# Performance work log

Measured on AMD Instinct MI355X. Metric: run time of the kernel, lower is better.

## Reference

```python
import jax, jax.numpy as jnp
import numpy as np

B, S, D_IN, D_OUT = 4, 2048, 1024, 64
USE_MASK = True

def setup_inputs() -> dict:
    key = jax.random.key(0)
    ks = jax.random.split(key, 6)
    return {
        "inputs_for_keys": jax.random.normal(ks[0], (B, S, D_IN), jnp.float32),
        "inputs_for_values": jax.random.normal(ks[1], (B, S, D_IN), jnp.float32),
        "inputs_for_queries": jax.random.normal(ks[2], (B, S, D_IN), jnp.float32),
        "Weight_Q": jax.random.normal(ks[3], (D_IN, D_OUT), jnp.float32) * 0.02,
        "Weight_K": jax.random.normal(ks[4], (D_IN, D_OUT), jnp.float32) * 0.02,
        "Weight_V": jax.random.normal(ks[5], (D_IN, D_OUT), jnp.float32) * 0.02,
    }

def reference(inputs_for_keys, inputs_for_values, inputs_for_queries, Weight_Q, Weight_K, Weight_V):
    Q = jnp.einsum('bsd,de->bse', inputs_for_queries, Weight_Q)
    K = jnp.einsum('bsd,de->bse', inputs_for_keys, Weight_K)
    V = jnp.einsum('bsd,de->bse', inputs_for_values, Weight_V)
    # scores: [B, S_q, S_k], scaled by sqrt(d_out)
    scores = jnp.einsum('bqe,bke->bqk', Q, K) / np.sqrt(D_OUT).astype(np.float32)
    if USE_MASK:
        # -inf strictly above the diagonal (causal mask), matching
        # transpose(tril(ones*-inf, -1)) in the original.
        q_idx = jnp.arange(S)[:, None]
        k_idx = jnp.arange(S)[None, :]
        scores = jnp.where(k_idx > q_idx, -jnp.inf, scores)
    attn = jax.nn.softmax(scores, axis=-1)
    return jnp.einsum('bqk,bke->bqe', attn, V)
```

## Files before the change

### kernel.cpp

```cpp
#include <hip/hip_runtime.h>
#include <hip/hip_bf16.h>
#include <stdint.h>

typedef __bf16 bf16_t;
typedef __bf16 bf16x8 __attribute__((ext_vector_type(8)));
typedef float f32x4 __attribute__((ext_vector_type(4)));

#define L2E 1.44269504088896340736f

static __device__ __forceinline__ f32x4 mfma16(bf16x8 a, bf16x8 b, f32x4 c) {
  return __builtin_amdgcn_mfma_f32_16x16x32_bf16(a, b, c, 0, 0, 0);
}

static __device__ __forceinline__ void gload_lds16(const void* g, void* l) {
  __builtin_amdgcn_global_load_lds(
      (const __attribute__((address_space(1))) uint32_t*)g,
      (__attribute__((address_space(3))) uint32_t*)l, 16, 0, 0);
}

static __device__ __forceinline__ float bf2f(uint16_t u) {
  union { uint32_t i; float f; } v; v.i = (uint32_t)u << 16; return v.f;
}

__global__ __launch_bounds__(256) void wt_kernel(const float* __restrict__ Wq,
                                                 const float* __restrict__ Wk,
                                                 const float* __restrict__ Wv,
                                                 bf16_t* __restrict__ Wt) {
  int gid = blockIdx.x * 256 + threadIdx.x;
  int proj = gid >> 16;
  int rem = gid & 65535;
  int k = rem >> 6, n = rem & 63;
  const float* W = (proj == 0) ? Wq : (proj == 1) ? Wk : Wv;
  float v = W[rem];
  if (proj == 0) v *= 0.125f;
  Wt[proj * 65536 + n * 1024 + k] = (bf16_t)v;
}

__global__ __launch_bounds__(512) void proj_kernel(
    const float* __restrict__ Xq, const float* __restrict__ Xk, const float* __restrict__ Xv,
    const bf16_t* __restrict__ Wt,
    bf16_t* __restrict__ Qb, bf16_t* __restrict__ Kb, bf16_t* __restrict__ Vt) {
  __shared__ alignas(16) char Xl[8 * 4096];
  __shared__ alignas(16) bf16_t Msm[8][16][64];

  int tid = threadIdx.x;
  int w = tid >> 6, lane = tid & 63;
  int l15 = lane & 15, g = lane >> 4;
  char* myx = Xl + w * 4096;
  int kw = w;

  bf16x8 Wf[4][4];

  auto loadW = [&](int p) {
    const char* wb = (const char*)Wt + (size_t)p * 131072 + (size_t)kw * 256;
#pragma unroll
    for (int ct = 0; ct < 4; ++ct) {
#pragma unroll
      for (int i = 0; i < 4; ++i) {
        int n = i * 4 + (lane >> 4);
        int srcb = ((lane & 15) * 16) ^ ((n & 7) << 4);
        gload_lds16(wb + (size_t)(ct * 16 + n) * 2048 + srcb, myx + i * 1024);
      }
      asm volatile("s_waitcnt vmcnt(0)" ::: "memory");
      __builtin_amdgcn_sched_barrier(0);
#pragma unroll
      for (int s2 = 0; s2 < 4; ++s2)
        Wf[ct][s2] = *(const bf16x8*)(myx + l15 * 256 + ((s2 * 64 + g * 16) ^ ((l15 & 7) << 4)));
      asm volatile("s_waitcnt lgkmcnt(0)" ::: "memory");
      __builtin_amdgcn_sched_barrier(0);
    }
  };

  f32x4 acc[4] = {};
  float4 xA[4], xB[4];

  auto issueX = [&](int t, int sub, float4* xr) {
    int p = t >> 9, lt = t & 511;
    const float* X = (p == 0) ? Xq : (p == 1) ? Xk : Xv;
    const float* base = X + (size_t)lt * 16384 + kw * 128 + sub * 64 + (lane & 15) * 4;
#pragma unroll
    for (int i = 0; i < 4; ++i)
      xr[i] = *(const float4*)(base + ((lane >> 4) + 4 * i) * 1024);
  };

  auto writeX = [&](const float4* xr, int sub) {
    char* buf = myx + sub * 2048;
#pragma unroll
    for (int i = 0; i < 4; ++i) {
      int rw = (lane >> 4) + 4 * i;
      bf16_t t4[4] = {(bf16_t)xr[i].x, (bf16_t)xr[i].y, (bf16_t)xr[i].z, (bf16_t)xr[i].w};
      *(uint2*)(buf + rw * 128 + (((lane & 15) * 8) ^ ((rw & 7) << 4))) = *(const uint2*)t4;
    }
    asm volatile("s_waitcnt lgkmcnt(0)" ::: "memory");
    __builtin_amdgcn_sched_barrier(0);
  };

  auto computeX = [&](int sub) {
    const char* buf = myx + sub * 2048;
#pragma unroll
    for (int ks = 0; ks < 2; ++ks) {
      bf16x8 af = *(const bf16x8*)(buf + l15 * 128 + ((ks * 64 + g * 16) ^ ((l15 & 7) << 4)));
#pragma unroll
      for (int ct = 0; ct < 4; ++ct)
        acc[ct] = mfma16(af, Wf[ct][sub * 2 + ks], acc[ct]);
    }
  };

  int t0 = blockIdx.x * 6;
  int cur_p = t0 >> 9;
  loadW(cur_p);
  issueX(t0, 0, xA);

#pragma unroll 1
  for (int T = 0; T < 6; ++T) {
    int t = t0 + T;
    int p = t >> 9, lt = t & 511;
    if (p != cur_p) { loadW(p); cur_p = p; }
    issueX(t, 1, xB);
    writeX(xA, 0);
    computeX(0);
    if (T < 5) issueX(t + 1, 0, xA);
    writeX(xB, 1);
    computeX(1);

#pragma unroll
    for (int ct = 0; ct < 4; ++ct)
#pragma unroll
      for (int r = 0; r < 4; ++r)
        Msm[w][g * 4 + r][ct * 16 + l15] = (bf16_t)acc[ct][r];
#pragma unroll
    for (int ct = 0; ct < 4; ++ct) acc[ct] = (f32x4){0.f, 0.f, 0.f, 0.f};
    __syncthreads();

    int row = tid >> 5, c0 = (tid & 31) * 2;
    float s0 = 0.f, s1 = 0.f;
#pragma unroll
    for (int w2 = 0; w2 < 8; ++w2) {
      uint32_t u = *(const uint32_t*)&Msm[w2][row][c0];
      s0 += bf2f((uint16_t)u);
      s1 += bf2f((uint16_t)(u >> 16));
    }

    if (p < 2) {
      bf16_t* Ob = (p == 0) ? Qb : Kb;
      bf16_t o2[2] = {(bf16_t)s0, (bf16_t)s1};
      *(uint32_t*)&Ob[(size_t)(lt * 16 + row) * 64 + c0] = *(const uint32_t*)o2;
      __syncthreads();
    } else {
      __syncthreads();
      bf16_t* Vsm = (bf16_t*)&Msm[0][0][0];
      bf16_t o2[2] = {(bf16_t)s0, (bf16_t)s1};
      *(uint32_t*)&Vsm[row * 72 + c0] = *(const uint32_t*)o2;
      __syncthreads();
      if (tid < 128) {
        int d = tid >> 1, h = tid & 1;
        int b = lt >> 7;
        int s_ = (lt & 127) * 16 + h * 8;
        bf16_t tmp[8];
#pragma unroll
        for (int i = 0; i < 8; ++i) tmp[i] = Vsm[(h * 8 + i) * 72 + d];
        *(uint4*)(Vt + ((size_t)(b * 64 + d)) * 2048 + s_) = *(const uint4*)tmp;
      }
      __syncthreads();
    }
  }
}

#define NW 8
__global__ __launch_bounds__(512) void attn_kernel(
    const bf16_t* __restrict__ Qb, const bf16_t* __restrict__ Kb,
    const bf16_t* __restrict__ Vt, float* __restrict__ Out) {
  __shared__ alignas(16) char Psm[NW * 2048];
  __shared__ float accL[NW][16][64];
  __shared__ float mL[NW][16];
  __shared__ float lL[NW][16];

  int b = blockIdx.y;
  int x = blockIdx.x;
  int qt = (b >= 2) ? (127 - x) : x;
  int q0 = qt * 16;
  int tid = threadIdx.x;
  int w = tid >> 6, lane = tid & 63;
  int l15 = lane & 15, g = lane >> 4;
  char* Pw = Psm + w * 2048;

  size_t qrow = (size_t)(b * 2048 + q0 + l15) * 64;
  bf16x8 qf0 = *(const bf16x8*)(Qb + qrow + g * 8);
  bf16x8 qf1 = *(const bf16x8*)(Qb + qrow + 32 + g * 8);

  float m_run[4] = {-1e30f, -1e30f, -1e30f, -1e30f};
  float l_run[4] = {0.f, 0.f, 0.f, 0.f};
  f32x4 acc_o[4] = {};

  int ntiles = (q0 + 79) >> 6;
  const bf16_t* kbase = Kb + (size_t)b * 2048 * 64;
  const bf16_t* vbase = Vt + (size_t)b * 64 * 2048;

  for (int t = w; t < ntiles; t += NW) {
    int kv0 = t * 64;
    f32x4 s[4] = {};
#pragma unroll
    for (int ct = 0; ct < 4; ++ct) {
      const bf16_t* kr = kbase + (size_t)(kv0 + ct * 16 + l15) * 64 + g * 8;
      s[ct] = mfma16(qf0, *(const bf16x8*)kr, s[ct]);
      s[ct] = mfma16(qf1, *(const bf16x8*)(kr + 32), s[ct]);
    }
    if (t == ntiles - 1) {
#pragma unroll
      for (int ct = 0; ct < 4; ++ct)
#pragma unroll
        for (int r = 0; r < 4; ++r) {
          int kg_ = kv0 + ct * 16 + l15;
          int qg_ = q0 + g * 4 + r;
          if (kg_ > qg_) s[ct][r] = -1e30f;
        }
    }

#pragma unroll
    for (int r = 0; r < 4; ++r) {
      float mx = fmaxf(fmaxf(s[0][r], s[1][r]), fmaxf(s[2][r], s[3][r]));
      mx = fmaxf(mx, __shfl_xor(mx, 1, 64));
      mx = fmaxf(mx, __shfl_xor(mx, 2, 64));
      mx = fmaxf(mx, __shfl_xor(mx, 4, 64));
      mx = fmaxf(mx, __shfl_xor(mx, 8, 64));
      float mnew = fmaxf(m_run[r], mx);
      float scale = exp2f((m_run[r] - mnew) * L2E);
      m_run[r] = mnew;
      float ps = 0.f;
      int qrl = g * 4 + r;
      char* pb = Pw + qrl * 128;
      int swp = (qrl & 7) << 4;
#pragma unroll
      for (int ct = 0; ct < 4; ++ct) {
        float p = exp2f((s[ct][r] - mnew) * L2E);
        ps += p;
        *(bf16_t*)(pb + ((ct * 32 + l15 * 2) ^ swp)) = (bf16_t)p;
      }
      ps += __shfl_xor(ps, 1, 64);
      ps += __shfl_xor(ps, 2, 64);
      ps += __shfl_xor(ps, 4, 64);
      ps += __shfl_xor(ps, 8, 64);
      l_run[r] = l_run[r] * scale + ps;
#pragma unroll
      for (int dt = 0; dt < 4; ++dt) acc_o[dt][r] *= scale;
    }

    int swpr = (l15 & 7) << 4;
#pragma unroll
    for (int ks = 0; ks < 2; ++ks) {
      bf16x8 pf = *(const bf16x8*)(Pw + l15 * 128 + ((ks * 64 + g * 16) ^ swpr));
#pragma unroll
      for (int dt = 0; dt < 4; ++dt) {
        const bf16_t* vr = vbase + (size_t)(dt * 16 + l15) * 2048 + kv0 + ks * 32 + g * 8;
        acc_o[dt] = mfma16(pf, *(const bf16x8*)vr, acc_o[dt]);
      }
    }
  }

  if (l15 == 0) {
#pragma unroll
    for (int r = 0; r < 4; ++r) {
      mL[w][g * 4 + r] = m_run[r];
      lL[w][g * 4 + r] = l_run[r];
    }
  }
#pragma unroll
  for (int dt = 0; dt < 4; ++dt)
#pragma unroll
    for (int r = 0; r < 4; ++r)
      accL[w][g * 4 + r][dt * 16 + l15] = acc_o[dt][r];
  __syncthreads();

  int row = tid >> 5, d0 = (tid & 31) * 2;
  float M = -1e30f;
#pragma unroll
  for (int w2 = 0; w2 < NW; ++w2) M = fmaxf(M, mL[w2][row]);
  float L = 0.f, o0 = 0.f, o1 = 0.f;
#pragma unroll
  for (int w2 = 0; w2 < NW; ++w2) {
    float sc = exp2f((mL[w2][row] - M) * L2E);
    L += lL[w2][row] * sc;
    o0 += sc * accL[w2][row][d0];
    o1 += sc * accL[w2][row][d0 + 1];
  }
  float inv = 1.0f / L;
  float2 o2 = {o0 * inv, o1 * inv};
  *(float2*)&Out[(size_t)(b * 2048 + q0 + row) * 64 + d0] = o2;
}

extern "C" void kernel_launch(void* const* d_in, const int* in_sizes, int n_in,
                              void* d_out, int out_size, void* d_ws, size_t ws_size,
                              hipStream_t stream) {
  const float* Xk = (const float*)d_in[0];
  const float* Xv = (const float*)d_in[1];
  const float* Xq = (const float*)d_in[2];
  const float* Wq = (const float*)d_in[3];
  const float* Wk = (const float*)d_in[4];
  const float* Wv = (const float*)d_in[5];
  float* Out = (float*)d_out;

  bf16_t* ws = (bf16_t*)d_ws;
  bf16_t* Qb = ws;
  bf16_t* Kb = ws + 524288;
  bf16_t* Vt = ws + 1048576;
  bf16_t* Wt = ws + 1572864;

  wt_kernel<<<dim3(768), dim3(256), 0, stream>>>(Wq, Wk, Wv, Wt);
  proj_kernel<<<dim3(256), dim3(512), 0, stream>>>(Xq, Xk, Xv, Wt, Qb, Kb, Vt);
  attn_kernel<<<dim3(128, 4), dim3(512), 0, stream>>>(Qb, Kb, Vt, Out);
}
```

Before: 53.24 us.

## Double attention query tile to 32 rows and halve projection tiles per block

The attention kernel now handles 32 query rows per block as two 16-row halves, so each K and V fragment loaded from global memory feeds two MFMAs. This halves redundant K/V traffic and halves the grid to 64x4 blocks, at the cost of more registers and LDS per block. The projection kernel runs 3 tiles per block over 512 blocks instead of 6 over 256, for more parallelism. The final merge across waves uses float4 loads and stores.

```diff
diff --git a/kernel.cpp b/kernel.cpp
--- a/kernel.cpp
+++ b/kernel.cpp
@@ -106,20 +106,20 @@
     }
   };
 
-  int t0 = blockIdx.x * 6;
+  int t0 = blockIdx.x * 3;
   int cur_p = t0 >> 9;
   loadW(cur_p);
   issueX(t0, 0, xA);
 
 #pragma unroll 1
-  for (int T = 0; T < 6; ++T) {
+  for (int T = 0; T < 3; ++T) {
     int t = t0 + T;
     int p = t >> 9, lt = t & 511;
     if (p != cur_p) { loadW(p); cur_p = p; }
     issueX(t, 1, xB);
     writeX(xA, 0);
     computeX(0);
-    if (T < 5) issueX(t + 1, 0, xA);
+    if (T < 2) issueX(t + 1, 0, xA);
     writeX(xB, 1);
     computeX(1);
 
@@ -170,122 +170,146 @@
 __global__ __launch_bounds__(512) void attn_kernel(
     const bf16_t* __restrict__ Qb, const bf16_t* __restrict__ Kb,
     const bf16_t* __restrict__ Vt, float* __restrict__ Out) {
-  __shared__ alignas(16) char Psm[NW * 2048];
-  __shared__ float accL[NW][16][64];
-  __shared__ float mL[NW][16];
-  __shared__ float lL[NW][16];
+  __shared__ alignas(16) char Psm[NW * 4096];
+  __shared__ float accL[NW][32][64];
+  __shared__ float mL[NW][32];
+  __shared__ float lL[NW][32];
 
   int b = blockIdx.y;
   int x = blockIdx.x;
-  int qt = (b >= 2) ? (127 - x) : x;
-  int q0 = qt * 16;
+  int qt = (b >= 2) ? (63 - x) : x;
+  int q0 = qt * 32;
   int tid = threadIdx.x;
   int w = tid >> 6, lane = tid & 63;
   int l15 = lane & 15, g = lane >> 4;
-  char* Pw = Psm + w * 2048;
-
-  size_t qrow = (size_t)(b * 2048 + q0 + l15) * 64;
-  bf16x8 qf0 = *(const bf16x8*)(Qb + qrow + g * 8);
-  bf16x8 qf1 = *(const bf16x8*)(Qb + qrow + 32 + g * 8);
-
-  float m_run[4] = {-1e30f, -1e30f, -1e30f, -1e30f};
-  float l_run[4] = {0.f, 0.f, 0.f, 0.f};
-  f32x4 acc_o[4] = {};
-
-  int ntiles = (q0 + 79) >> 6;
+  char* Pw = Psm + w * 4096;
+
+  bf16x8 qf[2][2];
+#pragma unroll
+  for (int h = 0; h < 2; ++h) {
+    size_t qrow = (size_t)(b * 2048 + q0 + h * 16 + l15) * 64;
+    qf[h][0] = *(const bf16x8*)(Qb + qrow + g * 8);
+    qf[h][1] = *(const bf16x8*)(Qb + qrow + 32 + g * 8);
+  }
+
+  float m_run[2][4], l_run[2][4];
+  f32x4 acc_o[2][4] = {};
+#pragma unroll
+  for (int h = 0; h < 2; ++h)
+#pragma unroll
+    for (int r = 0; r < 4; ++r) { m_run[h][r] = -1e30f; l_run[h][r] = 0.f; }
+
+  int ntiles = (q0 + 95) >> 6;
   const bf16_t* kbase = Kb + (size_t)b * 2048 * 64;
   const bf16_t* vbase = Vt + (size_t)b * 64 * 2048;
 
   for (int t = w; t < ntiles; t += NW) {
     int kv0 = t * 64;
-    f32x4 s[4] = {};
+    f32x4 s[2][4] = {};
 #pragma unroll
     for (int ct = 0; ct < 4; ++ct) {
       const bf16_t* kr = kbase + (size_t)(kv0 + ct * 16 + l15) * 64 + g * 8;
-      s[ct] = mfma16(qf0, *(const bf16x8*)kr, s[ct]);
-      s[ct] = mfma16(qf1, *(const bf16x8*)(kr + 32), s[ct]);
+      bf16x8 kf0 = *(const bf16x8*)kr;
+      bf16x8 kf1 = *(const bf16x8*)(kr + 32);
+#pragma unroll
+      for (int h = 0; h < 2; ++h) {
+        s[h][ct] = mfma16(qf[h][0], kf0, s[h][ct]);
+        s[h][ct] = mfma16(qf[h][1], kf1, s[h][ct]);
+      }
     }
     if (t == ntiles - 1) {
 #pragma unroll
-      for (int ct = 0; ct < 4; ++ct)
-#pragma unroll
-        for (int r = 0; r < 4; ++r) {
-          int kg_ = kv0 + ct * 16 + l15;
-          int qg_ = q0 + g * 4 + r;
-          if (kg_ > qg_) s[ct][r] = -1e30f;
+      for (int h = 0; h < 2; ++h)
+#pragma unroll
+        for (int ct = 0; ct < 4; ++ct)
+#pragma unroll
+          for (int r = 0; r < 4; ++r) {
+            int kg_ = kv0 + ct * 16 + l15;
+            int qg_ = q0 + h * 16 + g * 4 + r;
+            if (kg_ > qg_) s[h][ct][r] = -1e30f;
+          }
+    }
+
+#pragma unroll
+    for (int h = 0; h < 2; ++h)
+#pragma unroll
+      for (int r = 0; r < 4; ++r) {
+        float mx = fmaxf(fmaxf(s[h][0][r], s[h][1][r]), fmaxf(s[h][2][r], s[h][3][r]));
+        mx = fmaxf(mx, __shfl_xor(mx, 1, 64));
+        mx = fmaxf(mx, __shfl_xor(mx, 2, 64));
+        mx = fmaxf(mx, __shfl_xor(mx, 4, 64));
+        mx = fmaxf(mx, __shfl_xor(mx, 8, 64));
+        float mnew = fmaxf(m_run[h][r], mx);
+        float scale = exp2f((m_run[h][r] - mnew) * L2E);
+        m_run[h][r] = mnew;
+        float ps = 0.f;
+        int qrl = h * 16 + g * 4 + r;
+        char* pb = Pw + qrl * 128;
+        int swp = (qrl & 7) << 4;
+#pragma unroll
+        for (int ct = 0; ct < 4; ++ct) {
+          float p = exp2f((s[h][ct][r] - mnew) * L2E);
+          ps += p;
+          *(bf16_t*)(pb + ((ct * 32 + l15 * 2) ^ swp)) = (bf16_t)p;
         }
-    }
-
-#pragma unroll
-    for (int r = 0; r < 4; ++r) {
-      float mx = fmaxf(fmaxf(s[0][r], s[1][r]), fmaxf(s[2][r], s[3][r]));
-      mx = fmaxf(mx, __shfl_xor(mx, 1, 64));
-      mx = fmaxf(mx, __shfl_xor(mx, 2, 64));
-      mx = fmaxf(mx, __shfl_xor(mx, 4, 64));
-      mx = fmaxf(mx, __shfl_xor(mx, 8, 64));
-      float mnew = fmaxf(m_run[r], mx);
-      float scale = exp2f((m_run[r] - mnew) * L2E);
-      m_run[r] = mnew;
-      float ps = 0.f;
-      int qrl = g * 4 + r;
-      char* pb = Pw + qrl * 128;
-      int swp = (qrl & 7) << 4;
-#pragma unroll
-      for (int ct = 0; ct < 4; ++ct) {
-        float p = exp2f((s[ct][r] - mnew) * L2E);
-        ps += p;
-        *(bf16_t*)(pb + ((ct * 32 + l15 * 2) ^ swp)) = (bf16_t)p;
-      }
-      ps += __shfl_xor(ps, 1, 64);
-      ps += __shfl_xor(ps, 2, 64);
-      ps += __shfl_xor(ps, 4, 64);
-      ps += __shfl_xor(ps, 8, 64);
-      l_run[r] = l_run[r] * scale + ps;
-#pragma unroll
-      for (int dt = 0; dt < 4; ++dt) acc_o[dt][r] *= scale;
-    }
+        ps += __shfl_xor(ps, 1, 64);
+        ps += __shfl_xor(ps, 2, 64);
+        ps += __shfl_xor(ps, 4, 64);
+        ps += __shfl_xor(ps, 8, 64);
+        l_run[h][r] = l_run[h][r] * scale + ps;
+#pragma unroll
+        for (int dt = 0; dt < 4; ++dt) acc_o[h][dt][r] *= scale;
+      }
 
     int swpr = (l15 & 7) << 4;
 #pragma unroll
     for (int ks = 0; ks < 2; ++ks) {
-      bf16x8 pf = *(const bf16x8*)(Pw + l15 * 128 + ((ks * 64 + g * 16) ^ swpr));
+      bf16x8 pf0 = *(const bf16x8*)(Pw + l15 * 128 + ((ks * 64 + g * 16) ^ swpr));
+      bf16x8 pf1 = *(const bf16x8*)(Pw + (16 + l15) * 128 + ((ks * 64 + g * 16) ^ swpr));
 #pragma unroll
       for (int dt = 0; dt < 4; ++dt) {
         const bf16_t* vr = vbase + (size_t)(dt * 16 + l15) * 2048 + kv0 + ks * 32 + g * 8;
-        acc_o[dt] = mfma16(pf, *(const bf16x8*)vr, acc_o[dt]);
+        bf16x8 vf = *(const bf16x8*)vr;
+        acc_o[0][dt] = mfma16(pf0, vf, acc_o[0][dt]);
+        acc_o[1][dt] = mfma16(pf1, vf, acc_o[1][dt]);
       }
     }
   }
 
   if (l15 == 0) {
 #pragma unroll
-    for (int r = 0; r < 4; ++r) {
-      mL[w][g * 4 + r] = m_run[r];
-      lL[w][g * 4 + r] = l_run[r];
-    }
-  }
-#pragma unroll
-  for (int dt = 0; dt < 4; ++dt)
-#pragma unroll
-    for (int r = 0; r < 4; ++r)
-      accL[w][g * 4 + r][dt * 16 + l15] = acc_o[dt][r];
+    for (int h = 0; h < 2; ++h)
+#pragma unroll
+      for (int r = 0; r < 4; ++r) {
+        mL[w][h * 16 + g * 4 + r] = m_run[h][r];
+        lL[w][h * 16 + g * 4 + r] = l_run[h][r];
+      }
+  }
+#pragma unroll
+  for (int h = 0; h < 2; ++h)
+#pragma unroll
+    for (int dt = 0; dt < 4; ++dt)
+#pragma unroll
+      for (int r = 0; r < 4; ++r)
+        accL[w][h * 16 + g * 4 + r][dt * 16 + l15] = acc_o[h][dt][r];
   __syncthreads();
 
-  int row = tid >> 5, d0 = (tid & 31) * 2;
+  int row = tid >> 4, c0 = (tid & 15) * 4;
   float M = -1e30f;
 #pragma unroll
   for (int w2 = 0; w2 < NW; ++w2) M = fmaxf(M, mL[w2][row]);
-  float L = 0.f, o0 = 0.f, o1 = 0.f;
+  float L = 0.f;
+  f32x4 o = {0.f, 0.f, 0.f, 0.f};
 #pragma unroll
   for (int w2 = 0; w2 < NW; ++w2) {
     float sc = exp2f((mL[w2][row] - M) * L2E);
     L += lL[w2][row] * sc;
-    o0 += sc * accL[w2][row][d0];
-    o1 += sc * accL[w2][row][d0 + 1];
+    f32x4 a = *(const f32x4*)&accL[w2][row][c0];
+    o[0] += sc * a[0]; o[1] += sc * a[1]; o[2] += sc * a[2]; o[3] += sc * a[3];
   }
   float inv = 1.0f / L;
-  float2 o2 = {o0 * inv, o1 * inv};
-  *(float2*)&Out[(size_t)(b * 2048 + q0 + row) * 64 + d0] = o2;
+  float4 o4 = {o[0] * inv, o[1] * inv, o[2] * inv, o[3] * inv};
+  *(float4*)&Out[(size_t)(b * 2048 + q0 + row) * 64 + c0] = o4;
 }
 
 extern "C" void kernel_launch(void* const* d_in, const int* in_sizes, int n_in,
@@ -306,6 +330,6 @@
   bf16_t* Wt = ws + 1572864;
 
   wt_kernel<<<dim3(768), dim3(256), 0, stream>>>(Wq, Wk, Wv, Wt);
-  proj_kernel<<<dim3(256), dim3(512), 0, stream>>>(Xq, Xk, Xv, Wt, Qb, Kb, Vt);
-  attn_kernel<<<dim3(128, 4), dim3(512), 0, stream>>>(Qb, Kb, Vt, Out);
-}
+  proj_kernel<<<dim3(512), dim3(512), 0, stream>>>(Xq, Xk, Xv, Wt, Qb, Kb, Vt);
+  attn_kernel<<<dim3(64, 4), dim3(512), 0, stream>>>(Qb, Kb, Vt, Out);
+}
```

New measurement: 52.86 us. No clear change (-0.7%).
